# Kernel optimization log

Measured on AMD Instinct MI355X. Metric: run time of the kernel, lower is better.

The kernel has to match this reference:

```python
import jax, jax.numpy as jnp
import numpy as np

N, E, D_IN, D_E, D, L, D_OUT = 20000, 320000, 64, 16, 256, 4, 10


def _gine(x, e, src, dst, eps, W1, b1, W2, b2):
    """GINE conv: MLP((1+eps)*x + sum_{j->i} relu(x_j + e_ji))."""
    msg = jax.nn.relu(x[src] + e)                                   # [E, D]
    agg = jax.ops.segment_sum(msg, dst, num_segments=x.shape[0])    # [N, D]
    h = (1.0 + eps) * x + agg
    return jax.nn.relu(h @ W1 + b1) @ W2 + b2


def setup_inputs() -> dict:
    key = jax.random.key(0)
    ks = jax.random.split(key, 24)
    p = lambda k, sh: jax.random.normal(k, sh, jnp.float32) * 0.05
    return {
        "x": jax.random.normal(ks[0], (N, D_IN), jnp.float32),
        "edge_attr": jax.random.normal(ks[1], (E, D_E), jnp.float32),
        "edge_index": jax.random.randint(ks[2], (2, E), 0, N, jnp.int32),
        # FeatureEncoder: node and edge linear encoders to dim_inner
        "W_ne": p(ks[3], (D_IN, D)), "b_ne": jnp.zeros((D,), jnp.float32),
        "W_ee": p(ks[4], (D_E, D)), "b_ee": jnp.zeros((D,), jnp.float32),
        # pre-MP: one Linear+ReLU layer
        "W_pre": p(ks[5], (D, D)), "b_pre": jnp.zeros((D,), jnp.float32),
        # GINEAggregation (k-hop agg module)
        "eps_a": jnp.zeros((), jnp.float32),
        "W1_a": p(ks[6], (D, D)), "b1_a": jnp.zeros((D,), jnp.float32),
        "W2_a": p(ks[7], (D, D)), "b2_a": jnp.zeros((D,), jnp.float32),
        # L stacked DelayGINEConvLayer params
        "eps_l": jnp.zeros((L,), jnp.float32),
        "W1_l": p(ks[8], (L, D, D)), "b1_l": jnp.zeros((L, D), jnp.float32),
        "W2_l": p(ks[9], (L, D, D)), "b2_l": jnp.zeros((L, D), jnp.float32),
        # head
        "W_h": p(ks[10], (D, D_OUT)), "b_h": jnp.zeros((D_OUT,), jnp.float32),
    }


def reference(x, edge_attr, edge_index, W_ne, b_ne, W_ee, b_ee, W_pre, b_pre,
              eps_a, W1_a, b1_a, W2_a, b2_a, eps_l, W1_l, b1_l, W2_l, b2_l,
              W_h, b_h):
    src, dst = edge_index[0], edge_index[1]
    # FeatureEncoder
    h = x @ W_ne + b_ne                                  # [N, D]
    e = edge_attr @ W_ee + b_ee                          # [E, D]
    # pre-MP
    h = jax.nn.relu(h @ W_pre + b_pre)
    # k-hop GINE aggregation module
    h = _gine(h, e, src, dst, eps_a, W1_a, b1_a, W2_a, b2_a)
    # stacked DelayGINE conv layers with residual connections
    for i in range(L):
        h = h + _gine(h, e, src, dst, eps_l[i], W1_l[i], b1_l[i], W2_l[i], b2_l[i])
    # node-level head
    return h @ W_h + b_h                                 # [N, D_OUT]
```

## Files before the change

### kernel.cpp

```cpp
#include <hip/hip_runtime.h>
#include <hip/hip_bf16.h>

namespace {

constexpr int NN = 20000;
constexpr int NE = 320000;
constexpr int DI = 64;
constexpr int DE = 16;
constexpr int DM = 256;
constexpr int DO = 10;

__host__ __device__ constexpr size_t woff(int m) {
  return m == 0 ? 0 : (size_t)16384 + (size_t)(m - 1) * 65536;
}
constexpr size_t WTOTAL = 16384 + 11 * 65536;

typedef __attribute__((ext_vector_type(8))) short s16x8;
typedef __attribute__((ext_vector_type(4))) float f32x4;

__device__ inline unsigned short f2bf(float x) {
  union { float f; unsigned u; } c; c.f = x;
  unsigned r = (c.u + 0x7FFFu + ((c.u >> 16) & 1u)) >> 16;
  return (unsigned short)r;
}
__device__ inline float bf2f(unsigned short h) {
  union { unsigned u; float f; } c; c.u = ((unsigned)h) << 16;
  return c.f;
}

__device__ inline unsigned char f2e4m3(float x) {
  union { float f; unsigned u; } c; c.f = x;
  const unsigned s = (c.u >> 24) & 0x80u;
  c.u &= 0x7FFFFFFFu;
  c.f = fminf(c.f, 448.f);
  const unsigned b = c.u + 0x7FFFFu + ((c.u >> 20) & 1u);
  unsigned r = (b >> 20) - 960u;
  r = (c.f >= 0.0078125f) ? r : 0u;
  return (unsigned char)(s | r);
}
__device__ inline float e4m32f(unsigned u) {
  unsigned b = ((u & 0x80u) << 24) | (((u & 0x7Fu) << 20) + 0x3C000000u);
  if ((u & 0x7Fu) == 0) b &= 0x80000000u;
  union { unsigned u; float f; } c; c.u = b;
  return c.f;
}


__global__ __launch_bounds__(256) void hist_kernel(
    const int* __restrict__ dst, int* __restrict__ counts, int E)
{
  const int j = blockIdx.x * 256 + threadIdx.x;
  if (j < E) atomicAdd(&counts[dst[j]], 1);
}

__global__ __launch_bounds__(1024) void scan_kernel(
    const int* __restrict__ counts, int* __restrict__ row_ptr,
    int* __restrict__ cursor, int n)
{
  __shared__ int partial[1024];
  const int t = threadIdx.x;
  const int chunk = (n + 1023) / 1024;
  const int beg = t * chunk;
  const int end = min(beg + chunk, n);
  int s = 0;
  for (int i = beg; i < end; ++i) s += counts[i];
  partial[t] = s;
  __syncthreads();
  for (int off = 1; off < 1024; off <<= 1) {
    const int v = (t >= off) ? partial[t - off] : 0;
    __syncthreads();
    partial[t] += v;
    __syncthreads();
  }
  int base = (t == 0) ? 0 : partial[t - 1];
  for (int i = beg; i < end; ++i) {
    const int c = counts[i];
    row_ptr[i] = base;
    cursor[i] = base;
    base += c;
  }
  if (t == 1023) row_ptr[n] = partial[1023];
}

__global__ __launch_bounds__(256) void scatter_kernel(
    const int* __restrict__ src, const int* __restrict__ dst,
    const float* __restrict__ eattr, int* __restrict__ cursor,
    int* __restrict__ esrc, unsigned short* __restrict__ ea16, int E)
{
  const int j = blockIdx.x * 256 + threadIdx.x;
  if (j < E) {
    const int p = atomicAdd(&cursor[dst[j]], 1);
    esrc[p] = src[j];
    const float4* ep = reinterpret_cast<const float4*>(&eattr[(size_t)j * DE]);
    const float4 e0 = ep[0], e1 = ep[1], e2 = ep[2], e3 = ep[3];
    const float ea[16] = {e0.x, e0.y, e0.z, e0.w, e1.x, e1.y, e1.z, e1.w,
                          e2.x, e2.y, e2.z, e2.w, e3.x, e3.y, e3.z, e3.w};
    s16x8 v0, v1;
    #pragma unroll
    for (int k = 0; k < 8; ++k) {
      v0[k] = (short)f2bf(ea[k]);
      v1[k] = (short)f2bf(ea[8 + k]);
    }
    s16x8* op = reinterpret_cast<s16x8*>(&ea16[(size_t)p * DE]);
    op[0] = v0; op[1] = v1;
  }
}

__global__ __launch_bounds__(256) void convertW_kernel(
    const float* __restrict__ W_ne, const float* __restrict__ W_pre,
    const float* __restrict__ W1_a, const float* __restrict__ W2_a,
    const float* __restrict__ W1_l, const float* __restrict__ W2_l,
    unsigned short* __restrict__ hi, unsigned short* __restrict__ lo)
{
  const int mat = blockIdx.y;
  const float* src;
  int K = 256;
  if (mat == 0)      { src = W_ne;  K = 64; }
  else if (mat == 1) { src = W_pre; }
  else if (mat == 2) { src = W1_a; }
  else if (mat == 3) { src = W2_a; }
  else if (mat < 8)  { src = W1_l + (size_t)(mat - 4) * 65536; }
  else               { src = W2_l + (size_t)(mat - 8) * 65536; }
  const size_t off = woff(mat);

  const int ntiles = (K >> 6) * 4;
  const int t = blockIdx.x;
  if (t >= ntiles) return;
  const int tk = t % (K >> 6);
  const int tn = t / (K >> 6);

  __shared__ float tile[64][65];
  const int tid = threadIdx.x;
  const int c = tid & 63;
  const int rg = tid >> 6;
  for (int i = 0; i < 16; ++i) {
    const int r = rg + i * 4;
    tile[r][c] = src[(size_t)(tk * 64 + r) * 256 + tn * 64 + c];
  }
  __syncthreads();
  const int k = tk * 64 + c;
  for (int i = 0; i < 16; ++i) {
    const int nn = rg + i * 4;
    const int n = tn * 64 + nn;
    const float x = tile[c][nn];
    const unsigned short hh = f2bf(x);
    hi[off + (size_t)n * K + k] = hh;
    lo[off + (size_t)n * K + k] = f2bf(x - bf2f(hh));
  }
}

__global__ __launch_bounds__(256) void convertWee_kernel(
    const float* __restrict__ Wee, unsigned short* __restrict__ Wt16)
{
  const int n = threadIdx.x;
  #pragma unroll
  for (int k = 0; k < DE; ++k)
    Wt16[n * DE + k] = f2bf(Wee[k * DM + n]);
}

__global__ __launch_bounds__(256) void eenc_kernel(
    const unsigned short* __restrict__ ea16, const unsigned short* __restrict__ Wt16,
    const float* __restrict__ bee, unsigned char* __restrict__ e8)
{
  __shared__ unsigned char stage[128][144];
  const int tid = threadIdx.x;
  const int lane = tid & 63, wid = tid >> 6;
  const int l15 = lane & 15, l4 = lane >> 4;
  const int eBase0 = blockIdx.x * 128;
  const int eBase = eBase0 + wid * 32;
  const int colBase = blockIdx.y * 128;
  const s16x8 zz = {0, 0, 0, 0, 0, 0, 0, 0};

  s16x8 ah[2];
  #pragma unroll
  for (int mi = 0; mi < 2; ++mi) {
    const int edge = eBase + mi * 16 + l15;
    ah[mi] = (l4 < 2)
        ? *reinterpret_cast<const s16x8*>(&ea16[(size_t)edge * DE + l4 * 8]) : zz;
  }
  s16x8 bh[8];
  #pragma unroll
  for (int ni = 0; ni < 8; ++ni) {
    const int col = colBase + ni * 16 + l15;
    bh[ni] = (l4 < 2)
        ? *reinterpret_cast<const s16x8*>(&Wt16[col * DE + l4 * 8]) : zz;
  }
  f32x4 acc[2][8];
  #pragma unroll
  for (int mi = 0; mi < 2; ++mi)
    #pragma unroll
    for (int ni = 0; ni < 8; ++ni)
      acc[mi][ni] = (f32x4){0.f, 0.f, 0.f, 0.f};
  #pragma unroll
  for (int mi = 0; mi < 2; ++mi)
    #pragma unroll
    for (int ni = 0; ni < 8; ++ni)
      acc[mi][ni] = __builtin_amdgcn_mfma_f32_16x16x32_bf16(ah[mi], bh[ni], acc[mi][ni], 0, 0, 0);

  #pragma unroll
  for (int ni = 0; ni < 8; ++ni) {
    const int col = ni * 16 + l15;
    const float bv = bee[colBase + col];
    #pragma unroll
    for (int mi = 0; mi < 2; ++mi) {
      #pragma unroll
      for (int r = 0; r < 4; ++r) {
        const int erow = wid * 32 + mi * 16 + l4 * 4 + r;
        stage[erow][col] = f2e4m3(acc[mi][ni][r] + bv);
      }
    }
  }
  __syncthreads();
  #pragma unroll
  for (int it = 0; it < 4; ++it) {
    const int idx = tid + it * 256;
    const int e = idx >> 3, cc = idx & 7;
    const s16x8 v = *reinterpret_cast<const s16x8*>(&stage[e][cc * 16]);
    *reinterpret_cast<s16x8*>(&e8[(size_t)(eBase0 + e) * DM + colBase + cc * 16]) = v;
  }
}

template<bool RELU1, bool RELU2, bool RESID, bool ABF16>
__global__ __launch_bounds__(256) void mlp_kernel(
    const float* __restrict__ Af, const unsigned short* __restrict__ Ab,
    const unsigned short* __restrict__ B1h, const unsigned short* __restrict__ B1l,
    const float* __restrict__ b1,
    const unsigned short* __restrict__ B2h, const unsigned short* __restrict__ B2l,
    const float* __restrict__ b2,
    unsigned short* __restrict__ O16, int M, int K1)
{
  __shared__ unsigned short Tst[32 * 256];
  __shared__ unsigned short Wh[256 * 32], Wl[256 * 32];
  unsigned short* Ast = Tst;

  const int tid = threadIdx.x;
  const int lane = tid & 63, wid = tid >> 6;
  const int l15 = lane & 15, l4 = lane >> 4;
  const int rowBase = blockIdx.x * 32;
  const int colW = wid * 64;

  f32x4 acc[2][4];
  #pragma unroll
  for (int i = 0; i < 2; ++i)
    #pragma unroll
    for (int j = 0; j < 4; ++j) acc[i][j] = (f32x4){0.f, 0.f, 0.f, 0.f};

  const int nk1 = K1 >> 5;
  for (int ks = 0; ks < nk1; ++ks) {
    if (tid < 128) {
      const int row = tid >> 2, kc = tid & 3;
      const int grow = rowBase + row;
      const int chunk = row * 4 + (kc ^ ((row >> 1) & 3));
      s16x8 v = {0, 0, 0, 0, 0, 0, 0, 0};
      if (grow < M) {
        if (ABF16) {
          v = *reinterpret_cast<const s16x8*>(&Ab[(size_t)grow * K1 + ks * 32 + kc * 8]);
        } else {
          const float* p = Af + (size_t)grow * K1 + ks * 32 + kc * 8;
          const float4 v0 = *reinterpret_cast<const float4*>(p);
          const float4 v1 = *reinterpret_cast<const float4*>(p + 4);
          const float xs[8] = {v0.x, v0.y, v0.z, v0.w, v1.x, v1.y, v1.z, v1.w};
          #pragma unroll
          for (int j = 0; j < 8; ++j) v[j] = (short)f2bf(xs[j]);
        }
      }
      ((s16x8*)Ast)[chunk] = v;
    }
    #pragma unroll
    for (int i = 0; i < 4; ++i) {
      const int u = tid + i * 256;
      const int c = u >> 2, kc = u & 3;
      const int chunk = c * 4 + (kc ^ ((c >> 1) & 3));
      const size_t g = (size_t)c * K1 + ks * 32 + kc * 8;
      ((s16x8*)Wh)[chunk] = *reinterpret_cast<const s16x8*>(B1h + g);
      ((s16x8*)Wl)[chunk] = *reinterpret_cast<const s16x8*>(B1l + g);
    }
    __syncthreads();
    s16x8 a[2], bh[4], bl[4];
    #pragma unroll
    for (int mi = 0; mi < 2; ++mi) {
      const int r = mi * 16 + l15;
      a[mi] = ((const s16x8*)Ast)[r * 4 + (l4 ^ ((r >> 1) & 3))];
    }
    #pragma unroll
    for (int ni = 0; ni < 4; ++ni) {
      const int c = colW + ni * 16 + l15;
      const int ch = c * 4 + (l4 ^ ((c >> 1) & 3));
      bh[ni] = ((const s16x8*)Wh)[ch];
      bl[ni] = ((const s16x8*)Wl)[ch];
    }
    #pragma unroll
    for (int mi = 0; mi < 2; ++mi)
      #pragma unroll
      for (int ni = 0; ni < 4; ++ni) {
        acc[mi][ni] = __builtin_amdgcn_mfma_f32_16x16x32_bf16(a[mi], bh[ni], acc[mi][ni], 0, 0, 0);
        acc[mi][ni] = __builtin_amdgcn_mfma_f32_16x16x32_bf16(a[mi], bl[ni], acc[mi][ni], 0, 0, 0);
      }
    __syncthreads();
  }
  #pragma unroll
  for (int ni = 0; ni < 4; ++ni) {
    const int col = colW + ni * 16 + l15;
    const float bv = b1[col];
    #pragma unroll
    for (int mi = 0; mi < 2; ++mi) {
      #pragma unroll
      for (int r = 0; r < 4; ++r) {
        const int row = mi * 16 + l4 * 4 + r;
        float v = acc[mi][ni][r] + bv;
        if (RELU1) v = fmaxf(v, 0.f);
        const int c32 = col >> 3;
        const int chunk = row * 32 + (c32 ^ (row & 31));
        Tst[chunk * 8 + (col & 7)] = f2bf(v);
        acc[mi][ni][r] = 0.f;
      }
    }
  }
  __syncthreads();

  for (int ks = 0; ks < 8; ++ks) {
    #pragma unroll
    for (int i = 0; i < 4; ++i) {
      const int u = tid + i * 256;
      const int c = u >> 2, kc = u & 3;
      const int chunk = c * 4 + (kc ^ ((c >> 1) & 3));
      const size_t g = (size_t)c * 256 + ks * 32 + kc * 8;
      ((s16x8*)Wh)[chunk] = *reinterpret_cast<const s16x8*>(B2h + g);
      ((s16x8*)Wl)[chunk] = *reinterpret_cast<const s16x8*>(B2l + g);
    }
    __syncthreads();
    s16x8 a[2], bh[4], bl[4];
    #pragma unroll
    for (int mi = 0; mi < 2; ++mi) {
      const int row = mi * 16 + l15;
      const int c32 = ks * 4 + l4;
      a[mi] = ((const s16x8*)Tst)[row * 32 + (c32 ^ (row & 31))];
    }
    #pragma unroll
    for (int ni = 0; ni < 4; ++ni) {
      const int c = colW + ni * 16 + l15;
      const int ch = c * 4 + (l4 ^ ((c >> 1) & 3));
      bh[ni] = ((const s16x8*)Wh)[ch];
      bl[ni] = ((const s16x8*)Wl)[ch];
    }
    #pragma unroll
    for (int mi = 0; mi < 2; ++mi)
      #pragma unroll
      for (int ni = 0; ni < 4; ++ni) {
        acc[mi][ni] = __builtin_amdgcn_mfma_f32_16x16x32_bf16(a[mi], bh[ni], acc[mi][ni], 0, 0, 0);
        acc[mi][ni] = __builtin_amdgcn_mfma_f32_16x16x32_bf16(a[mi], bl[ni], acc[mi][ni], 0, 0, 0);
      }
    __syncthreads();
  }
  #pragma unroll
  for (int ni = 0; ni < 4; ++ni) {
    const int gcol = colW + ni * 16 + l15;
    const float bv = b2[gcol];
    #pragma unroll
    for (int mi = 0; mi < 2; ++mi) {
      #pragma unroll
      for (int r = 0; r < 4; ++r) {
        const int grow = rowBase + mi * 16 + l4 * 4 + r;
        if (grow < M) {
          float v = acc[mi][ni][r] + bv;
          if (RESID) v += bf2f(O16[(size_t)grow * DM + gcol]);
          if (RELU2) v = fmaxf(v, 0.f);
          O16[(size_t)grow * DM + gcol] = f2bf(v);
        }
      }
    }
  }
}

__global__ __launch_bounds__(256) void gather_e8_kernel(
    const unsigned short* __restrict__ h16,
    const int* __restrict__ row_ptr, const int* __restrict__ esrc,
    const unsigned char* __restrict__ e8,
    const float* __restrict__ eps_ptr, int eps_idx,
    unsigned short* __restrict__ out16, int n)
{
  const int tid = threadIdx.x;
  const int lane = tid & 63, wave = tid >> 6;
  const int half = lane >> 5;
  const int c8 = (lane & 31) * 8;
  const float ep1 = 1.0f + eps_ptr[eps_idx];
  const int stride = gridDim.x * 4;

  for (int i = blockIdx.x * 4 + wave; i < n; i += stride) {
    const int beg = row_ptr[i], end = row_ptr[i + 1];
    const int cnt = end - beg;
    float a[8];
    #pragma unroll
    for (int k = 0; k < 8; ++k) a[k] = 0.f;

    const int npair = cnt >> 1;
    int it = 0;
    for (; it + 4 <= npair; it += 4) {
      int pp[4], ss[4];
      #pragma unroll
      for (int j = 0; j < 4; ++j) {
        pp[j] = beg + 2 * (it + j) + half;
        ss[j] = esrc[pp[j]];
      }
      s16x8 hv[4]; uint2 ev[4];
      #pragma unroll
      for (int j = 0; j < 4; ++j) {
        hv[j] = *reinterpret_cast<const s16x8*>(&h16[(size_t)ss[j] * DM + c8]);
        ev[j] = *reinterpret_cast<const uint2*>(&e8[(size_t)pp[j] * DM + c8]);
      }
      #pragma unroll
      for (int j = 0; j < 4; ++j) {
        #pragma unroll
        for (int k = 0; k < 4; ++k) {
          a[k]     += fmaxf(bf2f((unsigned short)hv[j][k])     + e4m32f((ev[j].x >> (8 * k)) & 255u), 0.f);
          a[k + 4] += fmaxf(bf2f((unsigned short)hv[j][k + 4]) + e4m32f((ev[j].y >> (8 * k)) & 255u), 0.f);
        }
      }
    }
    for (; it < npair; ++it) {
      const int p0 = beg + 2 * it + half;
      const int s0 = esrc[p0];
      const s16x8 h0 = *reinterpret_cast<const s16x8*>(&h16[(size_t)s0 * DM + c8]);
      const uint2 e0 = *reinterpret_cast<const uint2*>(&e8[(size_t)p0 * DM + c8]);
      #pragma unroll
      for (int k = 0; k < 4; ++k) {
        a[k]     += fmaxf(bf2f((unsigned short)h0[k])     + e4m32f((e0.x >> (8 * k)) & 255u), 0.f);
        a[k + 4] += fmaxf(bf2f((unsigned short)h0[k + 4]) + e4m32f((e0.y >> (8 * k)) & 255u), 0.f);
      }
    }
    if ((cnt & 1) && half == 0) {
      const int p0 = end - 1;
      const int s0 = esrc[p0];
      const s16x8 h0 = *reinterpret_cast<const s16x8*>(&h16[(size_t)s0 * DM + c8]);
      const uint2 e0 = *reinterpret_cast<const uint2*>(&e8[(size_t)p0 * DM + c8]);
      #pragma unroll
      for (int k = 0; k < 4; ++k) {
        a[k]     += fmaxf(bf2f((unsigned short)h0[k])     + e4m32f((e0.x >> (8 * k)) & 255u), 0.f);
        a[k + 4] += fmaxf(bf2f((unsigned short)h0[k + 4]) + e4m32f((e0.y >> (8 * k)) & 255u), 0.f);
      }
    }
    #pragma unroll
    for (int k = 0; k < 8; ++k) a[k] += __shfl_xor(a[k], 32, 64);
    if (half == 0) {
      const s16x8 hs = *reinterpret_cast<const s16x8*>(&h16[(size_t)i * DM + c8]);
      s16x8 o;
      #pragma unroll
      for (int k = 0; k < 8; ++k)
        o[k] = (short)f2bf(ep1 * bf2f((unsigned short)hs[k]) + a[k]);
      *reinterpret_cast<s16x8*>(&out16[(size_t)i * DM + c8]) = o;
    }
  }
}

__global__ __launch_bounds__(256) void gather_rc_kernel(
    const unsigned short* __restrict__ h16,
    const int* __restrict__ row_ptr, const int* __restrict__ esrc,
    const unsigned short* __restrict__ ea16,
    const float* __restrict__ Wee, const float* __restrict__ bee,
    const float* __restrict__ eps_ptr, int eps_idx,
    unsigned short* __restrict__ out16, int n)
{
  const int tid = threadIdx.x;
  const int lane = tid & 63, wave = tid >> 6;
  const int c4 = lane * 4;
  float4 w[16];
  #pragma unroll
  for (int k = 0; k < 16; ++k)
    w[k] = *reinterpret_cast<const float4*>(&Wee[k * DM + c4]);
  const float4 bv = *reinterpret_cast<const float4*>(&bee[c4]);
  const float ep1 = 1.0f + eps_ptr[eps_idx];
  const int stride = gridDim.x * 4;

  for (int i = blockIdx.x * 4 + wave; i < n; i += stride) {
    const int beg = row_ptr[i], end = row_ptr[i + 1];
    float a0 = 0.f, a1 = 0.f, a2 = 0.f, a3 = 0.f;
    for (int p = beg; p < end; ++p) {
      const int s = esrc[p];
      const ushort4 hv = *reinterpret_cast<const ushort4*>(&h16[(size_t)s * DM + c4]);
      const s16x8* eap = reinterpret_cast<const s16x8*>(&ea16[(size_t)p * DE]);
      const s16x8 ew0 = eap[0], ew1 = eap[1];
      float m0 = bf2f(hv.x) + bv.x, m1 = bf2f(hv.y) + bv.y;
      float m2 = bf2f(hv.z) + bv.z, m3 = bf2f(hv.w) + bv.w;
      float ea[16];
      #pragma unroll
      for (int k = 0; k < 8; ++k) {
        ea[k] = bf2f((unsigned short)ew0[k]);
        ea[8 + k] = bf2f((unsigned short)ew1[k]);
      }
      #pragma unroll
      for (int k = 0; k < 16; ++k) {
        m0 += ea[k] * w[k].x; m1 += ea[k] * w[k].y;
        m2 += ea[k] * w[k].z; m3 += ea[k] * w[k].w;
      }
      a0 += fmaxf(m0, 0.f); a1 += fmaxf(m1, 0.f);
      a2 += fmaxf(m2, 0.f); a3 += fmaxf(m3, 0.f);
    }
    const ushort4 hs = *reinterpret_cast<const ushort4*>(&h16[(size_t)i * DM + c4]);
    ushort4 o;
    o.x = f2bf(ep1 * bf2f(hs.x) + a0); o.y = f2bf(ep1 * bf2f(hs.y) + a1);
    o.z = f2bf(ep1 * bf2f(hs.z) + a2); o.w = f2bf(ep1 * bf2f(hs.w) + a3);
    *reinterpret_cast<ushort4*>(&out16[(size_t)i * DM + c4]) = o;
  }
}

__global__ __launch_bounds__(256) void head_kernel(
    const unsigned short* __restrict__ h16, const float* __restrict__ W,
    const float* __restrict__ b, float* __restrict__ out, int M)
{
  __shared__ float Ws[DM * DO];
  const int tid = threadIdx.x;
  for (int i = tid; i < DM * DO; i += 256) Ws[i] = W[i];
  __syncthreads();
  const int r = tid >> 4;
  const int c = tid & 15;
  const int row = blockIdx.x * 16 + r;
  if (row < M && c < DO) {
    const unsigned short* hp = &h16[(size_t)row * DM];
    float acc = 0.f;
    #pragma unroll 8
    for (int k = 0; k < DM; ++k) acc += bf2f(hp[k]) * Ws[k * DO + c];
    out[(size_t)row * DO + c] = acc + b[c];
  }
}

}

extern "C" void kernel_launch(void* const* d_in, const int* in_sizes, int n_in,
                              void* d_out, int out_size, void* d_ws, size_t ws_size,
                              hipStream_t stream) {
  const float* x     = (const float*)d_in[0];
  const float* eattr = (const float*)d_in[1];
  const int*   eidx  = (const int*)d_in[2];
  const float* W_ne  = (const float*)d_in[3];
  const float* b_ne  = (const float*)d_in[4];
  const float* W_ee  = (const float*)d_in[5];
  const float* b_ee  = (const float*)d_in[6];
  const float* W_pre = (const float*)d_in[7];
  const float* b_pre = (const float*)d_in[8];
  const float* eps_a = (const float*)d_in[9];
  const float* W1_a  = (const float*)d_in[10];
  const float* b1_a  = (const float*)d_in[11];
  const float* W2_a  = (const float*)d_in[12];
  const float* b2_a  = (const float*)d_in[13];
  const float* eps_l = (const float*)d_in[14];
  const float* W1_l  = (const float*)d_in[15];
  const float* b1_l  = (const float*)d_in[16];
  const float* W2_l  = (const float*)d_in[17];
  const float* b2_l  = (const float*)d_in[18];
  const float* W_h   = (const float*)d_in[19];
  const float* b_h   = (const float*)d_in[20];

  const int* src = eidx;
  const int* dst = eidx + NE;

  char* wp = (char*)d_ws;
  unsigned short* h16   = (unsigned short*)wp; wp += (size_t)NN * DM * 2;
  unsigned short* agg16 = (unsigned short*)wp; wp += (size_t)NN * DM * 2;
  unsigned short* ea16  = (unsigned short*)wp; wp += (size_t)NE * DE * 2;
  unsigned short* wt_hi = (unsigned short*)wp; wp += WTOTAL * 2;
  unsigned short* wt_lo = (unsigned short*)wp; wp += WTOTAL * 2;
  unsigned short* wtee  = (unsigned short*)wp; wp += (size_t)DM * DE * 2;
  int* esrc    = (int*)wp;                     wp += (size_t)NE * 4;
  int* counts  = (int*)wp;                     wp += (size_t)NN * 4;
  int* row_ptr = (int*)wp;                     wp += (size_t)(NN + 1) * 4;
  int* cursor  = (int*)wp;                     wp += (size_t)NN * 4;
  wp = (char*)(((uintptr_t)wp + 15) & ~(uintptr_t)15);
  unsigned char* e8 = (unsigned char*)wp;
  const size_t need_e8 = (size_t)(wp - (char*)d_ws) + (size_t)NE * DM;
  const bool use_e8 = ws_size >= need_e8;

  hipMemsetAsync(counts, 0, NN * sizeof(int), stream);
  hist_kernel<<<(NE + 255) / 256, 256, 0, stream>>>(dst, counts, NE);
  scan_kernel<<<1, 1024, 0, stream>>>(counts, row_ptr, cursor, NN);
  scatter_kernel<<<(NE + 255) / 256, 256, 0, stream>>>(
      src, dst, eattr, cursor, esrc, ea16, NE);

  convertW_kernel<<<dim3(16, 12), 256, 0, stream>>>(
      W_ne, W_pre, W1_a, W2_a, W1_l, W2_l, wt_hi, wt_lo);
  convertWee_kernel<<<1, 256, 0, stream>>>(W_ee, wtee);

  if (use_e8)
    eenc_kernel<<<dim3(NE / 128, 2), 256, 0, stream>>>(ea16, wtee, b_ee, e8);

  const int mlpgrid = (NN + 31) / 32;

  mlp_kernel<false, true, false, false><<<mlpgrid, 256, 0, stream>>>(
      x, nullptr,
      wt_hi + woff(0), wt_lo + woff(0), b_ne,
      wt_hi + woff(1), wt_lo + woff(1), b_pre,
      h16, NN, DI);

  for (int layer = 0; layer < 5; ++layer) {
    const float* eps; int ei; const float *b1, *b2; size_t o1, o2;
    if (layer == 0) {
      eps = eps_a; ei = 0; b1 = b1_a; b2 = b2_a;
      o1 = woff(2); o2 = woff(3);
    } else {
      const int i = layer - 1;
      eps = eps_l; ei = i;
      b1 = b1_l + (size_t)i * DM; b2 = b2_l + (size_t)i * DM;
      o1 = woff(4 + i); o2 = woff(8 + i);
    }
    if (use_e8)
      gather_e8_kernel<<<5000, 256, 0, stream>>>(
          h16, row_ptr, esrc, e8, eps, ei, agg16, NN);
    else
      gather_rc_kernel<<<1280, 256, 0, stream>>>(
          h16, row_ptr, esrc, ea16, W_ee, b_ee, eps, ei, agg16, NN);
    if (layer == 0)
      mlp_kernel<true, false, false, true><<<mlpgrid, 256, 0, stream>>>(
          nullptr, agg16, wt_hi + o1, wt_lo + o1, b1,
          wt_hi + o2, wt_lo + o2, b2, h16, NN, DM);
    else
      mlp_kernel<true, false, true, true><<<mlpgrid, 256, 0, stream>>>(
          nullptr, agg16, wt_hi + o1, wt_lo + o1, b1,
          wt_hi + o2, wt_lo + o2, b2, h16, NN, DM);
  }

  head_kernel<<<(NN + 15) / 16, 256, 0, stream>>>(h16, W_h, b_h, (float*)d_out, NN);
}
```

Before: 514.4 us.

## Drop bf16 hi/lo weight split and enlarge MLP tiles to 64 rows

Weights are now converted to a single bf16 copy rather than a hi+lo pair, which halves the MFMA count and the weight traffic in the fused MLP kernel. The MLP kernel also moves to 512 threads covering 64 rows per block, so each weight tile staged in shared memory is reused across twice as many rows. The swizzle pattern changes to match, and the counts memset becomes a small kernel. The cost is lower weight precision, since the bf16 rounding error of the weights is no longer corrected.

```diff
diff --git a/kernel.cpp b/kernel.cpp
--- a/kernel.cpp
+++ b/kernel.cpp
@@ -45,6 +45,11 @@
   return c.f;
 }
 
+
+__global__ __launch_bounds__(256) void zero_kernel(int* __restrict__ p, int n) {
+  const int j = blockIdx.x * 256 + threadIdx.x;
+  if (j < n) p[j] = 0;
+}
 
 __global__ __launch_bounds__(256) void hist_kernel(
     const int* __restrict__ dst, int* __restrict__ counts, int E)
@@ -110,7 +115,7 @@
     const float* __restrict__ W_ne, const float* __restrict__ W_pre,
     const float* __restrict__ W1_a, const float* __restrict__ W2_a,
     const float* __restrict__ W1_l, const float* __restrict__ W2_l,
-    unsigned short* __restrict__ hi, unsigned short* __restrict__ lo)
+    unsigned short* __restrict__ hi)
 {
   const int mat = blockIdx.y;
   const float* src;
@@ -142,10 +147,7 @@
   for (int i = 0; i < 16; ++i) {
     const int nn = rg + i * 4;
     const int n = tn * 64 + nn;
-    const float x = tile[c][nn];
-    const unsigned short hh = f2bf(x);
-    hi[off + (size_t)n * K + k] = hh;
-    lo[off + (size_t)n * K + k] = f2bf(x - bf2f(hh));
+    hi[off + (size_t)n * K + k] = f2bf(tile[c][nn]);
   }
 }
 
@@ -221,23 +223,22 @@
 }
 
 template<bool RELU1, bool RELU2, bool RESID, bool ABF16>
-__global__ __launch_bounds__(256) void mlp_kernel(
+__global__ __launch_bounds__(512) void mlp_kernel(
     const float* __restrict__ Af, const unsigned short* __restrict__ Ab,
-    const unsigned short* __restrict__ B1h, const unsigned short* __restrict__ B1l,
-    const float* __restrict__ b1,
-    const unsigned short* __restrict__ B2h, const unsigned short* __restrict__ B2l,
-    const float* __restrict__ b2,
+    const unsigned short* __restrict__ B1, const float* __restrict__ b1,
+    const unsigned short* __restrict__ B2, const float* __restrict__ b2,
     unsigned short* __restrict__ O16, int M, int K1)
 {
-  __shared__ unsigned short Tst[32 * 256];
-  __shared__ unsigned short Wh[256 * 32], Wl[256 * 32];
+  __shared__ unsigned short Tst[64 * 256];
+  __shared__ unsigned short Ws[256 * 32];
   unsigned short* Ast = Tst;
 
   const int tid = threadIdx.x;
   const int lane = tid & 63, wid = tid >> 6;
+  const int wr = wid >> 2, wc = wid & 3;
   const int l15 = lane & 15, l4 = lane >> 4;
-  const int rowBase = blockIdx.x * 32;
-  const int colW = wid * 64;
+  const int rowBase = blockIdx.x * 64;
+  const int colW = wc * 64;
 
   f32x4 acc[2][4];
   #pragma unroll
@@ -247,10 +248,10 @@
 
   const int nk1 = K1 >> 5;
   for (int ks = 0; ks < nk1; ++ks) {
-    if (tid < 128) {
+    if (tid < 256) {
       const int row = tid >> 2, kc = tid & 3;
       const int grow = rowBase + row;
-      const int chunk = row * 4 + (kc ^ ((row >> 1) & 3));
+      const int chunk = row * 4 + (kc ^ (row & 3));
       s16x8 v = {0, 0, 0, 0, 0, 0, 0, 0};
       if (grow < M) {
         if (ABF16) {
@@ -267,35 +268,29 @@
       ((s16x8*)Ast)[chunk] = v;
     }
     #pragma unroll
-    for (int i = 0; i < 4; ++i) {
-      const int u = tid + i * 256;
+    for (int i = 0; i < 2; ++i) {
+      const int u = tid + i * 512;
       const int c = u >> 2, kc = u & 3;
-      const int chunk = c * 4 + (kc ^ ((c >> 1) & 3));
-      const size_t g = (size_t)c * K1 + ks * 32 + kc * 8;
-      ((s16x8*)Wh)[chunk] = *reinterpret_cast<const s16x8*>(B1h + g);
-      ((s16x8*)Wl)[chunk] = *reinterpret_cast<const s16x8*>(B1l + g);
+      const int chunk = c * 4 + (kc ^ (c & 3));
+      ((s16x8*)Ws)[chunk] = *reinterpret_cast<const s16x8*>(B1 + (size_t)c * K1 + ks * 32 + kc * 8);
     }
     __syncthreads();
-    s16x8 a[2], bh[4], bl[4];
+    s16x8 a[2], bw[4];
     #pragma unroll
     for (int mi = 0; mi < 2; ++mi) {
-      const int r = mi * 16 + l15;
-      a[mi] = ((const s16x8*)Ast)[r * 4 + (l4 ^ ((r >> 1) & 3))];
+      const int r = wr * 32 + mi * 16 + l15;
+      a[mi] = ((const s16x8*)Ast)[r * 4 + (l4 ^ (r & 3))];
     }
     #pragma unroll
     for (int ni = 0; ni < 4; ++ni) {
       const int c = colW + ni * 16 + l15;
-      const int ch = c * 4 + (l4 ^ ((c >> 1) & 3));
-      bh[ni] = ((const s16x8*)Wh)[ch];
-      bl[ni] = ((const s16x8*)Wl)[ch];
+      bw[ni] = ((const s16x8*)Ws)[c * 4 + (l4 ^ (c & 3))];
     }
     #pragma unroll
     for (int mi = 0; mi < 2; ++mi)
       #pragma unroll
-      for (int ni = 0; ni < 4; ++ni) {
-        acc[mi][ni] = __builtin_amdgcn_mfma_f32_16x16x32_bf16(a[mi], bh[ni], acc[mi][ni], 0, 0, 0);
-        acc[mi][ni] = __builtin_amdgcn_mfma_f32_16x16x32_bf16(a[mi], bl[ni], acc[mi][ni], 0, 0, 0);
-      }
+      for (int ni = 0; ni < 4; ++ni)
+        acc[mi][ni] = __builtin_amdgcn_mfma_f32_16x16x32_bf16(a[mi], bw[ni], acc[mi][ni], 0, 0, 0);
     __syncthreads();
   }
   #pragma unroll
@@ -306,7 +301,7 @@
     for (int mi = 0; mi < 2; ++mi) {
       #pragma unroll
       for (int r = 0; r < 4; ++r) {
-        const int row = mi * 16 + l4 * 4 + r;
+        const int row = wr * 32 + mi * 16 + l4 * 4 + r;
         float v = acc[mi][ni][r] + bv;
         if (RELU1) v = fmaxf(v, 0.f);
         const int c32 = col >> 3;
@@ -320,36 +315,30 @@
 
   for (int ks = 0; ks < 8; ++ks) {
     #pragma unroll
-    for (int i = 0; i < 4; ++i) {
-      const int u = tid + i * 256;
+    for (int i = 0; i < 2; ++i) {
+      const int u = tid + i * 512;
       const int c = u >> 2, kc = u & 3;
-      const int chunk = c * 4 + (kc ^ ((c >> 1) & 3));
-      const size_t g = (size_t)c * 256 + ks * 32 + kc * 8;
-      ((s16x8*)Wh)[chunk] = *reinterpret_cast<const s16x8*>(B2h + g);
-      ((s16x8*)Wl)[chunk] = *reinterpret_cast<const s16x8*>(B2l + g);
+      const int chunk = c * 4 + (kc ^ (c & 3));
+      ((s16x8*)Ws)[chunk] = *reinterpret_cast<const s16x8*>(B2 + (size_t)c * 256 + ks * 32 + kc * 8);
     }
     __syncthreads();
-    s16x8 a[2], bh[4], bl[4];
+    s16x8 a[2], bw[4];
     #pragma unroll
     for (int mi = 0; mi < 2; ++mi) {
-      const int row = mi * 16 + l15;
+      const int row = wr * 32 + mi * 16 + l15;
       const int c32 = ks * 4 + l4;
       a[mi] = ((const s16x8*)Tst)[row * 32 + (c32 ^ (row & 31))];
     }
     #pragma unroll
     for (int ni = 0; ni < 4; ++ni) {
       const int c = colW + ni * 16 + l15;
-      const int ch = c * 4 + (l4 ^ ((c >> 1) & 3));
-      bh[ni] = ((const s16x8*)Wh)[ch];
-      bl[ni] = ((const s16x8*)Wl)[ch];
+      bw[ni] = ((const s16x8*)Ws)[c * 4 + (l4 ^ (c & 3))];
     }
     #pragma unroll
     for (int mi = 0; mi < 2; ++mi)
       #pragma unroll
-      for (int ni = 0; ni < 4; ++ni) {
-        acc[mi][ni] = __builtin_amdgcn_mfma_f32_16x16x32_bf16(a[mi], bh[ni], acc[mi][ni], 0, 0, 0);
-        acc[mi][ni] = __builtin_amdgcn_mfma_f32_16x16x32_bf16(a[mi], bl[ni], acc[mi][ni], 0, 0, 0);
-      }
+      for (int ni = 0; ni < 4; ++ni)
+        acc[mi][ni] = __builtin_amdgcn_mfma_f32_16x16x32_bf16(a[mi], bw[ni], acc[mi][ni], 0, 0, 0);
     __syncthreads();
   }
   #pragma unroll
@@ -360,7 +349,7 @@
     for (int mi = 0; mi < 2; ++mi) {
       #pragma unroll
       for (int r = 0; r < 4; ++r) {
-        const int grow = rowBase + mi * 16 + l4 * 4 + r;
+        const int grow = rowBase + wr * 32 + mi * 16 + l4 * 4 + r;
         if (grow < M) {
           float v = acc[mi][ni][r] + bv;
           if (RESID) v += bf2f(O16[(size_t)grow * DM + gcol]);
@@ -557,8 +546,7 @@
   unsigned short* h16   = (unsigned short*)wp; wp += (size_t)NN * DM * 2;
   unsigned short* agg16 = (unsigned short*)wp; wp += (size_t)NN * DM * 2;
   unsigned short* ea16  = (unsigned short*)wp; wp += (size_t)NE * DE * 2;
-  unsigned short* wt_hi = (unsigned short*)wp; wp += WTOTAL * 2;
-  unsigned short* wt_lo = (unsigned short*)wp; wp += WTOTAL * 2;
+  unsigned short* wt    = (unsigned short*)wp; wp += WTOTAL * 2;
   unsigned short* wtee  = (unsigned short*)wp; wp += (size_t)DM * DE * 2;
   int* esrc    = (int*)wp;                     wp += (size_t)NE * 4;
   int* counts  = (int*)wp;                     wp += (size_t)NN * 4;
@@ -569,26 +557,23 @@
   const size_t need_e8 = (size_t)(wp - (char*)d_ws) + (size_t)NE * DM;
   const bool use_e8 = ws_size >= need_e8;
 
-  hipMemsetAsync(counts, 0, NN * sizeof(int), stream);
+  zero_kernel<<<(NN + 255) / 256, 256, 0, stream>>>(counts, NN);
   hist_kernel<<<(NE + 255) / 256, 256, 0, stream>>>(dst, counts, NE);
   scan_kernel<<<1, 1024, 0, stream>>>(counts, row_ptr, cursor, NN);
   scatter_kernel<<<(NE + 255) / 256, 256, 0, stream>>>(
       src, dst, eattr, cursor, esrc, ea16, NE);
 
   convertW_kernel<<<dim3(16, 12), 256, 0, stream>>>(
-      W_ne, W_pre, W1_a, W2_a, W1_l, W2_l, wt_hi, wt_lo);
+      W_ne, W_pre, W1_a, W2_a, W1_l, W2_l, wt);
   convertWee_kernel<<<1, 256, 0, stream>>>(W_ee, wtee);
 
   if (use_e8)
     eenc_kernel<<<dim3(NE / 128, 2), 256, 0, stream>>>(ea16, wtee, b_ee, e8);
 
-  const int mlpgrid = (NN + 31) / 32;
-
-  mlp_kernel<false, true, false, false><<<mlpgrid, 256, 0, stream>>>(
-      x, nullptr,
-      wt_hi + woff(0), wt_lo + woff(0), b_ne,
-      wt_hi + woff(1), wt_lo + woff(1), b_pre,
-      h16, NN, DI);
+  const int mlpgrid = (NN + 63) / 64;
+
+  mlp_kernel<false, true, false, false><<<mlpgrid, 512, 0, stream>>>(
+      x, nullptr, wt + woff(0), b_ne, wt + woff(1), b_pre, h16, NN, DI);
 
   for (int layer = 0; layer < 5; ++layer) {
     const float* eps; int ei; const float *b1, *b2; size_t o1, o2;
@@ -608,13 +593,11 @@
       gather_rc_kernel<<<1280, 256, 0, stream>>>(
           h16, row_ptr, esrc, ea16, W_ee, b_ee, eps, ei, agg16, NN);
     if (layer == 0)
-      mlp_kernel<true, false, false, true><<<mlpgrid, 256, 0, stream>>>(
-          nullptr, agg16, wt_hi + o1, wt_lo + o1, b1,
-          wt_hi + o2, wt_lo + o2, b2, h16, NN, DM);
+      mlp_kernel<true, false, false, true><<<mlpgrid, 512, 0, stream>>>(
+          nullptr, agg16, wt + o1, b1, wt + o2, b2, h16, NN, DM);
     else
-      mlp_kernel<true, false, true, true><<<mlpgrid, 256, 0, stream>>>(
-          nullptr, agg16, wt_hi + o1, wt_lo + o1, b1,
-          wt_hi + o2, wt_lo + o2, b2, h16, NN, DM);
+      mlp_kernel<true, false, true, true><<<mlpgrid, 512, 0, stream>>>(
+          nullptr, agg16, wt + o1, b1, wt + o2, b2, h16, NN, DM);
   }
 
   head_kernel<<<(NN + 15) / 16, 256, 0, stream>>>(h16, W_h, b_h, (float*)d_out, NN);
```

Result: faster. 462.1 us (-10.2%).
